# Optimization experiments

Measured on AMD Instinct MI355X. Metric: run time of the kernel, lower is better.

## Reference

```python
import jax, jax.numpy as jnp
import numpy as np

NUM_HEADS = 8
LOGIT_MAX = float(np.log(1.0 / 0.01))  # log(100)


def setup_inputs() -> dict:
    key = jax.random.key(0)
    kq, kk, kv, kp = jax.random.split(key, 4)
    B, n, L, C = 16, 100, 64, 256
    return {
        "query": jax.random.normal(kq, (B, n, L, C), dtype=jnp.float32),
        "key": jax.random.normal(kk, (B, n, L, C), dtype=jnp.float32),
        "value": jax.random.normal(kv, (B, n, L, C), dtype=jnp.float32),
        "position": jax.random.normal(kp, (B, NUM_HEADS, L, L), dtype=jnp.float32),
        "logit_scale": jnp.full((NUM_HEADS, 1, 1), np.log(10.0), dtype=jnp.float32),
    }


def reference(query, key, value, position, logit_scale):
    B, n, Lq, C = query.shape
    Lv = key.shape[2]
    H = NUM_HEADS
    Dh = C // H
    q = query.reshape(B, n, Lq, H, Dh)
    k = key.reshape(B, n, Lv, H, Dh)
    v = value.reshape(B, n, Lv, H, Dh)
    # [B, n, H, Lq, Lv]
    attn = jnp.einsum("bnqhd,bnkhd->bnhqk", q, k)
    scale = jnp.exp(jnp.minimum(logit_scale, LOGIT_MAX))  # (H,1,1)
    attn = attn * scale + position[:, None]  # broadcast over window dim n
    attn = jax.nn.softmax(attn, axis=-1)
    x = jnp.einsum("bnhqk,bnkhd->bnqhd", attn, v).reshape(B, n, Lq, C)
    return (x, attn)
```

## Files before the change

### kernel.cpp

```cpp
#include <hip/hip_runtime.h>


typedef __attribute__((ext_vector_type(8))) short bf16x8;
typedef __attribute__((ext_vector_type(4))) float f32x4;

#define LOGIT_MAX_F 4.605170185988091f

__device__ __forceinline__ short f2bf(float f) {
    union { float f; unsigned u; } c; c.f = f;
    unsigned r = c.u + 0x7FFFu + ((c.u >> 16) & 1u);
    return (short)(r >> 16);
}
__device__ __forceinline__ float bf2f(short s) {
    union { unsigned u; float f; } c; c.u = ((unsigned)(unsigned short)s) << 16;
    return c.f;
}

#define VT_OFF 0
#define P_OFF  (32 * 72)
#define SMEM_SHORTS (32 * 72 + 64 * 72)

__device__ __forceinline__ f32x4 qk_tile(const float4 ka, const float4 kb2,
                                         const bf16x8 qh, const bf16x8 ql,
                                         f32x4 acc)
{
    const float kf[8] = {ka.x, ka.y, ka.z, ka.w, kb2.x, kb2.y, kb2.z, kb2.w};
    bf16x8 kh, kl;
    #pragma unroll
    for (int i = 0; i < 8; ++i) {
        const short hi = f2bf(kf[i]);
        kh[i] = hi;
        kl[i] = f2bf(kf[i] - bf2f(hi));
    }
    acc = __builtin_amdgcn_mfma_f32_16x16x32_bf16(qh, kh, acc, 0, 0, 0);
    acc = __builtin_amdgcn_mfma_f32_16x16x32_bf16(qh, kl, acc, 0, 0, 0);
    acc = __builtin_amdgcn_mfma_f32_16x16x32_bf16(ql, kh, acc, 0, 0, 0);
    return acc;
}

__global__ __launch_bounds__(256, 5) void tat_attn_kernel(
    const float* __restrict__ Qg, const float* __restrict__ Kg,
    const float* __restrict__ Vg, const float* __restrict__ Pg,
    const float* __restrict__ LSg,
    float* __restrict__ Xout, float* __restrict__ Aout)
{
    constexpr int L = 64, C = 256, H = 8, NW = 100;
    __shared__ short smem[SMEM_SHORTS];

    const int blk = blockIdx.x;
    const int h  = blk & 7;
    const int bw = blk >> 3;
    const int t  = threadIdx.x;
    const int wave = t >> 6;
    const int lane = t & 63;
    const int quad = lane >> 4;
    const int l15  = lane & 15;

    const float* qb = Qg + (size_t)bw * L * C + h * 32;
    const float* kb = Kg + (size_t)bw * L * C + h * 32;
    const float* vb = Vg + (size_t)bw * L * C + h * 32;
    const int b = bw / NW;
    const float* pb = Pg + (size_t)(b * H + h) * L * L;
    float* xb = Xout + (size_t)bw * L * C + h * 32;
    float* ab = Aout + ((size_t)bw * H + h) * L * L;

    const float scale = __expf(fminf(LSg[h], LOGIT_MAX_F));

    const float4 v0 = *(const float4*)(vb + lane * C + wave * 8);
    const float4 v1 = *(const float4*)(vb + lane * C + wave * 8 + 4);
    const int qrow = 16 * wave + l15;
    const float4 q0 = *(const float4*)(qb + qrow * C + quad * 8);
    const float4 q1 = *(const float4*)(qb + qrow * C + quad * 8 + 4);
    const float4 k0a = *(const float4*)(kb + l15 * C + quad * 8);
    const float4 k0b = *(const float4*)(kb + l15 * C + quad * 8 + 4);
    const float4 k1a = *(const float4*)(kb + (16 + l15) * C + quad * 8);
    const float4 k1b = *(const float4*)(kb + (16 + l15) * C + quad * 8 + 4);

    {
        const float va[8] = {v0.x, v0.y, v0.z, v0.w, v1.x, v1.y, v1.z, v1.w};
        #pragma unroll
        for (int i = 0; i < 8; ++i)
            smem[VT_OFF + (wave * 8 + i) * 72 + lane] = f2bf(va[i]);
    }

    bf16x8 qh, ql;
    {
        const float qa[8] = {q0.x, q0.y, q0.z, q0.w, q1.x, q1.y, q1.z, q1.w};
        #pragma unroll
        for (int i = 0; i < 8; ++i) {
            const short hi = f2bf(qa[i]);
            qh[i] = hi;
            ql[i] = f2bf(qa[i] - bf2f(hi));
        }
    }

    const float4 k2a = *(const float4*)(kb + (32 + l15) * C + quad * 8);
    const float4 k2b = *(const float4*)(kb + (32 + l15) * C + quad * 8 + 4);
    const float4 k3a = *(const float4*)(kb + (48 + l15) * C + quad * 8);
    const float4 k3b = *(const float4*)(kb + (48 + l15) * C + quad * 8 + 4);

    f32x4 acc0 = {0,0,0,0}, acc1 = {0,0,0,0}, acc2 = {0,0,0,0}, acc3 = {0,0,0,0};
    acc0 = qk_tile(k0a, k0b, qh, ql, acc0);
    acc1 = qk_tile(k1a, k1b, qh, ql, acc1);
    acc2 = qk_tile(k2a, k2b, qh, ql, acc2);
    acc3 = qk_tile(k3a, k3b, qh, ql, acc3);

    float lg[4][4];
    #pragma unroll
    for (int r = 0; r < 4; ++r) {
        const int row = 16 * wave + quad * 4 + r;
        const int cb  = row * L + l15;
        lg[0][r] = fmaf(acc0[r], scale, pb[cb + 0]);
        lg[1][r] = fmaf(acc1[r], scale, pb[cb + 16]);
        lg[2][r] = fmaf(acc2[r], scale, pb[cb + 32]);
        lg[3][r] = fmaf(acc3[r], scale, pb[cb + 48]);
    }

    float p[4][4];
    #pragma unroll
    for (int r = 0; r < 4; ++r) {
        float m = fmaxf(fmaxf(lg[0][r], lg[1][r]), fmaxf(lg[2][r], lg[3][r]));
        #pragma unroll
        for (int off = 8; off > 0; off >>= 1) m = fmaxf(m, __shfl_xor(m, off));
        const float e0 = __expf(lg[0][r] - m);
        const float e1 = __expf(lg[1][r] - m);
        const float e2 = __expf(lg[2][r] - m);
        const float e3 = __expf(lg[3][r] - m);
        float s = (e0 + e1) + (e2 + e3);
        #pragma unroll
        for (int off = 8; off > 0; off >>= 1) s += __shfl_xor(s, off);
        const float inv = 1.0f / s;
        p[0][r] = e0 * inv; p[1][r] = e1 * inv; p[2][r] = e2 * inv; p[3][r] = e3 * inv;
    }

    #pragma unroll
    for (int r = 0; r < 4; ++r) {
        const int row = 16 * wave + quad * 4 + r;
        #pragma unroll
        for (int t4 = 0; t4 < 4; ++t4) {
            const int col = 16 * t4 + l15;
            ab[row * L + col] = p[t4][r];
            smem[P_OFF + row * 72 + col] = f2bf(p[t4][r]);
        }
    }

    __syncthreads();

    f32x4 o0 = {0,0,0,0}, o1 = {0,0,0,0};
    #pragma unroll
    for (int hh = 0; hh < 2; ++hh) {
        const bf16x8 ap  = *(const bf16x8*)(smem + P_OFF + (16 * wave + l15) * 72 + hh * 32 + quad * 8);
        const bf16x8 bv0 = *(const bf16x8*)(smem + VT_OFF + l15 * 72        + hh * 32 + quad * 8);
        const bf16x8 bv1 = *(const bf16x8*)(smem + VT_OFF + (l15 + 16) * 72 + hh * 32 + quad * 8);
        o0 = __builtin_amdgcn_mfma_f32_16x16x32_bf16(ap, bv0, o0, 0, 0, 0);
        o1 = __builtin_amdgcn_mfma_f32_16x16x32_bf16(ap, bv1, o1, 0, 0, 0);
    }

    #pragma unroll
    for (int r = 0; r < 4; ++r) {
        const int row = 16 * wave + quad * 4 + r;
        xb[row * C + l15]      = o0[r];
        xb[row * C + 16 + l15] = o1[r];
    }
}

extern "C" void kernel_launch(void* const* d_in, const int* in_sizes, int n_in,
                              void* d_out, int out_size, void* d_ws, size_t ws_size,
                              hipStream_t stream) {
    const float* q   = (const float*)d_in[0];
    const float* k   = (const float*)d_in[1];
    const float* v   = (const float*)d_in[2];
    const float* pos = (const float*)d_in[3];
    const float* ls  = (const float*)d_in[4];
    float* out = (float*)d_out;

    constexpr int B = 16, NW = 100, L = 64, C = 256, H = 8;
    float* x_out = out;
    float* a_out = out + (size_t)B * NW * L * C;

    const int blocks = B * NW * H;
    tat_attn_kernel<<<blocks, 256, 0, stream>>>(q, k, v, pos, ls, x_out, a_out);
}
```

Before: 583.8 us.

## Stage K hi/lo bf16 split in LDS once per block, hoist position loads

Each K element is now loaded from global memory and split into hi/lo bf16 once per block by all 256 threads, then stored in shared memory. Before, each of the four waves loaded and converted all 64 K rows itself. The position loads are issued early into registers so their latency overlaps the conversion work. The barrier moves to before the QK MFMAs, and the one after the P write is dropped because each wave reads only its own P rows. This adds LDS traffic and raises shared memory use to about 24KB per block, in exchange for removing redundant global loads and redundant conversion ALU work.

```diff
diff --git a/kernel.cpp b/kernel.cpp
--- a/kernel.cpp
+++ b/kernel.cpp
@@ -16,27 +16,11 @@
     return c.f;
 }
 
-#define VT_OFF 0
-#define P_OFF  (32 * 72)
-#define SMEM_SHORTS (32 * 72 + 64 * 72)
-
-__device__ __forceinline__ f32x4 qk_tile(const float4 ka, const float4 kb2,
-                                         const bf16x8 qh, const bf16x8 ql,
-                                         f32x4 acc)
-{
-    const float kf[8] = {ka.x, ka.y, ka.z, ka.w, kb2.x, kb2.y, kb2.z, kb2.w};
-    bf16x8 kh, kl;
-    #pragma unroll
-    for (int i = 0; i < 8; ++i) {
-        const short hi = f2bf(kf[i]);
-        kh[i] = hi;
-        kl[i] = f2bf(kf[i] - bf2f(hi));
-    }
-    acc = __builtin_amdgcn_mfma_f32_16x16x32_bf16(qh, kh, acc, 0, 0, 0);
-    acc = __builtin_amdgcn_mfma_f32_16x16x32_bf16(qh, kl, acc, 0, 0, 0);
-    acc = __builtin_amdgcn_mfma_f32_16x16x32_bf16(ql, kh, acc, 0, 0, 0);
-    return acc;
-}
+#define KHI_OFF 0
+#define KLO_OFF 2560
+#define VT_OFF  5120
+#define P_OFF   7424
+#define SMEM_SHORTS 12032
 
 __global__ __launch_bounds__(256, 5) void tat_attn_kernel(
     const float* __restrict__ Qg, const float* __restrict__ Kg,
@@ -66,18 +50,43 @@
 
     const float scale = __expf(fminf(LSg[h], LOGIT_MAX_F));
 
+    const int r8 = t >> 2;
+    const int c8 = (t & 3) * 8;
+    const float4 k0 = *(const float4*)(kb + r8 * C + c8);
+    const float4 k1 = *(const float4*)(kb + r8 * C + c8 + 4);
+
     const float4 v0 = *(const float4*)(vb + lane * C + wave * 8);
     const float4 v1 = *(const float4*)(vb + lane * C + wave * 8 + 4);
+
     const int qrow = 16 * wave + l15;
     const float4 q0 = *(const float4*)(qb + qrow * C + quad * 8);
     const float4 q1 = *(const float4*)(qb + qrow * C + quad * 8 + 4);
-    const float4 k0a = *(const float4*)(kb + l15 * C + quad * 8);
-    const float4 k0b = *(const float4*)(kb + l15 * C + quad * 8 + 4);
-    const float4 k1a = *(const float4*)(kb + (16 + l15) * C + quad * 8);
-    const float4 k1b = *(const float4*)(kb + (16 + l15) * C + quad * 8 + 4);
+
+    float posr[4][4];
+    #pragma unroll
+    for (int r = 0; r < 4; ++r) {
+        const int cb = (16 * wave + quad * 4 + r) * L + l15;
+        posr[0][r] = pb[cb + 0];
+        posr[1][r] = pb[cb + 16];
+        posr[2][r] = pb[cb + 32];
+        posr[3][r] = pb[cb + 48];
+    }
 
     {
-        const float va[8] = {v0.x, v0.y, v0.z, v0.w, v1.x, v1.y, v1.z, v1.w};
+        const float ka[8] = {k0.x,k0.y,k0.z,k0.w,k1.x,k1.y,k1.z,k1.w};
+        bf16x8 kh, kl;
+        #pragma unroll
+        for (int i = 0; i < 8; ++i) {
+            const short hi = f2bf(ka[i]);
+            kh[i] = hi;
+            kl[i] = f2bf(ka[i] - bf2f(hi));
+        }
+        *(bf16x8*)(smem + KHI_OFF + r8 * 40 + c8) = kh;
+        *(bf16x8*)(smem + KLO_OFF + r8 * 40 + c8) = kl;
+    }
+
+    {
+        const float va[8] = {v0.x,v0.y,v0.z,v0.w,v1.x,v1.y,v1.z,v1.w};
         #pragma unroll
         for (int i = 0; i < 8; ++i)
             smem[VT_OFF + (wave * 8 + i) * 72 + lane] = f2bf(va[i]);
@@ -85,7 +94,7 @@
 
     bf16x8 qh, ql;
     {
-        const float qa[8] = {q0.x, q0.y, q0.z, q0.w, q1.x, q1.y, q1.z, q1.w};
+        const float qa[8] = {q0.x,q0.y,q0.z,q0.w,q1.x,q1.y,q1.z,q1.w};
         #pragma unroll
         for (int i = 0; i < 8; ++i) {
             const short hi = f2bf(qa[i]);
@@ -94,26 +103,27 @@
         }
     }
 
-    const float4 k2a = *(const float4*)(kb + (32 + l15) * C + quad * 8);
-    const float4 k2b = *(const float4*)(kb + (32 + l15) * C + quad * 8 + 4);
-    const float4 k3a = *(const float4*)(kb + (48 + l15) * C + quad * 8);
-    const float4 k3b = *(const float4*)(kb + (48 + l15) * C + quad * 8 + 4);
+    __syncthreads();
 
     f32x4 acc0 = {0,0,0,0}, acc1 = {0,0,0,0}, acc2 = {0,0,0,0}, acc3 = {0,0,0,0};
-    acc0 = qk_tile(k0a, k0b, qh, ql, acc0);
-    acc1 = qk_tile(k1a, k1b, qh, ql, acc1);
-    acc2 = qk_tile(k2a, k2b, qh, ql, acc2);
-    acc3 = qk_tile(k3a, k3b, qh, ql, acc3);
+    #pragma unroll
+    for (int t4 = 0; t4 < 4; ++t4) {
+        const bf16x8 bkh = *(const bf16x8*)(smem + KHI_OFF + (16*t4 + l15)*40 + quad*8);
+        const bf16x8 bkl = *(const bf16x8*)(smem + KLO_OFF + (16*t4 + l15)*40 + quad*8);
+        f32x4 a = (t4==0)?acc0:(t4==1)?acc1:(t4==2)?acc2:acc3;
+        a = __builtin_amdgcn_mfma_f32_16x16x32_bf16(qh, bkh, a, 0, 0, 0);
+        a = __builtin_amdgcn_mfma_f32_16x16x32_bf16(qh, bkl, a, 0, 0, 0);
+        a = __builtin_amdgcn_mfma_f32_16x16x32_bf16(ql, bkh, a, 0, 0, 0);
+        if (t4==0) acc0 = a; else if (t4==1) acc1 = a; else if (t4==2) acc2 = a; else acc3 = a;
+    }
 
     float lg[4][4];
     #pragma unroll
     for (int r = 0; r < 4; ++r) {
-        const int row = 16 * wave + quad * 4 + r;
-        const int cb  = row * L + l15;
-        lg[0][r] = fmaf(acc0[r], scale, pb[cb + 0]);
-        lg[1][r] = fmaf(acc1[r], scale, pb[cb + 16]);
-        lg[2][r] = fmaf(acc2[r], scale, pb[cb + 32]);
-        lg[3][r] = fmaf(acc3[r], scale, pb[cb + 48]);
+        lg[0][r] = fmaf(acc0[r], scale, posr[0][r]);
+        lg[1][r] = fmaf(acc1[r], scale, posr[1][r]);
+        lg[2][r] = fmaf(acc2[r], scale, posr[2][r]);
+        lg[3][r] = fmaf(acc3[r], scale, posr[3][r]);
     }
 
     float p[4][4];
@@ -144,14 +154,12 @@
         }
     }
 
-    __syncthreads();
-
     f32x4 o0 = {0,0,0,0}, o1 = {0,0,0,0};
     #pragma unroll
     for (int hh = 0; hh < 2; ++hh) {
-        const bf16x8 ap  = *(const bf16x8*)(smem + P_OFF + (16 * wave + l15) * 72 + hh * 32 + quad * 8);
-        const bf16x8 bv0 = *(const bf16x8*)(smem + VT_OFF + l15 * 72        + hh * 32 + quad * 8);
-        const bf16x8 bv1 = *(const bf16x8*)(smem + VT_OFF + (l15 + 16) * 72 + hh * 32 + quad * 8);
+        const bf16x8 ap  = *(const bf16x8*)(smem + P_OFF + (16*wave + l15)*72 + hh*32 + quad*8);
+        const bf16x8 bv0 = *(const bf16x8*)(smem + VT_OFF + l15*72        + hh*32 + quad*8);
+        const bf16x8 bv1 = *(const bf16x8*)(smem + VT_OFF + (l15+16)*72   + hh*32 + quad*8);
         o0 = __builtin_amdgcn_mfma_f32_16x16x32_bf16(ap, bv0, o0, 0, 0, 0);
         o1 = __builtin_amdgcn_mfma_f32_16x16x32_bf16(ap, bv1, o1, 0, 0, 0);
     }
```

Result: faster. 545.1 us (-6.6%).
